# Kernel optimization log

Hardware: AMD Instinct MI355X
Metric: run time of the kernel (lower is better)

The kernel has to match this reference:

```python
import jax, jax.numpy as jnp
import numpy as np

N = 65536      # nodes
E = 524288     # edges (avg degree 8)
C = 128        # in_channels == hidden_channels
L = 3          # num_layers
EPS = 1e-5     # BatchNorm eps


def setup_inputs() -> dict:
    key = jax.random.key(0)
    ks = jax.random.split(key, 12)
    inv = 1.0 / np.sqrt(C)
    return {
        "x": jax.random.normal(ks[0], (N, C), jnp.float32),
        "edge_weight": jax.random.uniform(ks[1], (E,), jnp.float32),
        "bn_gamma": 1.0 + 0.1 * jax.random.normal(ks[2], (L, C), jnp.float32),
        "bn_beta": 0.1 * jax.random.normal(ks[3], (L, C), jnp.float32),
        "W_self": inv * jax.random.normal(ks[4], (L, C, C), jnp.float32),
        "W_neigh": inv * jax.random.normal(ks[5], (L, C, C), jnp.float32),
        "bias": 0.01 * jax.random.normal(ks[6], (L, C), jnp.float32),
        "lin_w": inv * jax.random.normal(ks[7], (C,), jnp.float32),
        "lin_b": 0.01 * jax.random.normal(ks[8], (), jnp.float32),
        "src": jax.random.randint(ks[9], (E,), 0, N),
        "dst": jax.random.randint(ks[10], (E,), 0, N),
    }


def reference(x, edge_weight, bn_gamma, bn_beta, W_self, W_neigh, bias, lin_w, lin_b, src, dst):
    # log1p on edge weights (done once in the torch module per layer; identical each layer)
    ew = jnp.log1p(edge_weight)[:, None]                     # [E,1]
    # in-degree for mean aggregation (DGL fn.mean); isolated nodes -> divide by 1 (sum is 0)
    deg = jax.ops.segment_sum(jnp.ones((E,), x.dtype), dst, num_segments=N)
    deg = jnp.maximum(deg, 1.0)[:, None]                     # [N,1]

    h = x
    for l in range(L):
        # BatchNorm1d over nodes (training-mode batch stats, biased variance)
        mu = jnp.mean(h, axis=0)
        var = jnp.mean((h - mu) ** 2, axis=0)
        h = (h - mu) * jax.lax.rsqrt(var + EPS) * bn_gamma[l] + bn_beta[l]
        # SAGEConv mean aggregator: msg = h[src] * w, neigh = mean over in-edges
        msg = h[src] * ew                                    # [E,C]
        neigh = jax.ops.segment_sum(msg, dst, num_segments=N) / deg  # [N,C]
        h = jax.nn.relu(h @ W_self[l] + neigh @ W_neigh[l] + bias[l])
    return h @ lin_w + lin_b                                 # [N]
```

## Files before the change

### kernel.cpp

```cpp
#include <hip/hip_runtime.h>
#include <hip/hip_fp16.h>

#define NN 65536
#define EE 524288
#define CC 128
#define CAP 32

typedef _Float16 f16x8 __attribute__((ext_vector_type(8)));
typedef float f32x4 __attribute__((ext_vector_type(4)));


__global__ void k_init(const float* __restrict__ x, __half* __restrict__ h,
                       float* __restrict__ pstat0,
                       const int* __restrict__ src, const int* __restrict__ dst,
                       const float* __restrict__ ew,
                       int* __restrict__ cnt, unsigned int* __restrict__ buf) {
    int b = blockIdx.x, t = threadIdx.x;
    if (b < 256) {
        const float4* xv = (const float4*)x;
        __half2* o = (__half2*)h;
        float s[4] = {0, 0, 0, 0}, q[4] = {0, 0, 0, 0};
        for (int k = 0; k < 32; k++) {
            int i = b * 8192 + k * 256 + t;
            float4 v = xv[i];
            o[2 * i]     = __floats2half2_rn(v.x, v.y);
            o[2 * i + 1] = __floats2half2_rn(v.z, v.w);
            s[0] += v.x; s[1] += v.y; s[2] += v.z; s[3] += v.w;
            q[0] += v.x * v.x; q[1] += v.y * v.y; q[2] += v.z * v.z; q[3] += v.w * v.w;
        }
        __shared__ float ls[256];
        ls[t] = 0.f;
        __syncthreads();
        int c0 = (t & 31) * 4;
#pragma unroll
        for (int u = 0; u < 4; u++) {
            atomicAdd(&ls[c0 + u], s[u]);
            atomicAdd(&ls[128 + c0 + u], q[u]);
        }
        __syncthreads();
        if (t < 128) {
            atomicAdd(&pstat0[t], ls[t]);
            atomicAdd(&pstat0[128 + t], ls[128 + t]);
        }
    } else {
        int base = (b - 256) * 1024 + t;
        int dd[4], sr[4];
        float we[4];
#pragma unroll
        for (int u = 0; u < 4; u++) dd[u] = dst[base + u * 256];
#pragma unroll
        for (int u = 0; u < 4; u++) sr[u] = src[base + u * 256];
#pragma unroll
        for (int u = 0; u < 4; u++) we[u] = ew[base + u * 256];
        int pos[4];
#pragma unroll
        for (int u = 0; u < 4; u++) pos[u] = atomicAdd(&cnt[dd[u]], 1);
#pragma unroll
        for (int u = 0; u < 4; u++) {
            float w = log1pf(we[u]);
            unsigned int pk = (unsigned int)sr[u] |
                              ((unsigned int)__half_as_ushort(__float2half(w)) << 16);
            if (pos[u] < CAP) buf[dd[u] * CAP + pos[u]] = pk;
        }
    }
}


__global__ void k_fold(const float* __restrict__ pstat_l,
                       const float* __restrict__ gamma, const float* __restrict__ beta,
                       const float* __restrict__ Ws, const float* __restrict__ Wn,
                       const float* __restrict__ bias,
                       __half* __restrict__ Wcat, float* __restrict__ crow,
                       float* __restrict__ cneigh) {
    int bid = blockIdx.x;
    int tid = threadIdx.x;
    int c = bid * 2 + (tid >> 7);
    int k = tid & 127;
    float mu = pstat_l[k] * (1.0f / NN);
    float var = pstat_l[128 + k] * (1.0f / NN) - mu * mu;
    float alpha = rsqrtf(var + 1e-5f) * gamma[k];
    float delta = beta[k] - mu * alpha;
    float ws = Ws[k * 128 + c];
    float wn = Wn[k * 128 + c];
    Wcat[c * 256 + k]       = __float2half(alpha * ws);
    Wcat[c * 256 + 128 + k] = __float2half(alpha * wn);
    float rs = delta * ws, rn = delta * wn;
#pragma unroll
    for (int off = 1; off < 64; off <<= 1) {
        rs += __shfl_xor(rs, off);
        rn += __shfl_xor(rn, off);
    }
    __shared__ float tmp[8];
    int wv = tid >> 6;
    if ((tid & 63) == 0) { tmp[wv * 2] = rs; tmp[wv * 2 + 1] = rn; }
    __syncthreads();
    if ((tid & 127) == 0) {
        int base = (tid >> 7) * 4;
        crow[c]   = bias[c] + tmp[base + 0] + tmp[base + 2];
        cneigh[c] = tmp[base + 1] + tmp[base + 3];
    }
}

__launch_bounds__(256, 4)
__global__ void k_layer(const __half* __restrict__ hin,
                        const int* __restrict__ cnt,
                        const unsigned int* __restrict__ buf,
                        const __half* __restrict__ Wcat,
                        const float* __restrict__ crow, const float* __restrict__ cneigh,
                        float* __restrict__ sod, int writeSod,
                        const float* __restrict__ lin_w, const float* __restrict__ lin_b,
                        __half* __restrict__ hout, float* __restrict__ outv, int mode,
                        float* __restrict__ pstatN) {
    __shared__ __half aggT[128 * 136];
    __shared__ float sodT[128];
    int tid = threadIdx.x;
    int lane = tid & 63;
    int wvid = tid >> 6;
    int l15 = lane & 15, quad = lane >> 4;
    int i0 = blockIdx.x * 128;
    int rbase = i0 + wvid * 32;

    f16x8 as0[4], as1[4];
#pragma unroll
    for (int s = 0; s < 4; s++) {
        int kof = s * 32 + quad * 8;
        as0[s] = *(const f16x8*)&hin[(rbase + l15) * 128 + kof];
        as1[s] = *(const f16x8*)&hin[(rbase + 16 + l15) * 128 + kof];
    }

    const __half2* h2 = (const __half2*)hin;
    int dv = 0;
    if (lane < 32) { dv = cnt[rbase + lane]; if (dv > CAP) dv = CAP; }
    int dA = __shfl(dv, 0), dB = __shfl(dv, 1);
    unsigned int pkA = 0, pkB = 0;
    if (lane < dA) pkA = buf[(rbase + 0) * CAP + lane];
    if (lane < dB) pkB = buf[(rbase + 1) * CAP + lane];

    for (int pair = 0; pair < 16; ++pair) {
        int ndA = 0, ndB = 0;
        unsigned int npA = 0, npB = 0;
        if (pair < 15) {
            ndA = __shfl(dv, 2 * pair + 2);
            ndB = __shfl(dv, 2 * pair + 3);
            if (lane < ndA) npA = buf[(rbase + 2 * pair + 2) * CAP + lane];
            if (lane < ndB) npB = buf[(rbase + 2 * pair + 3) * CAP + lane];
        }
        float ax[8], ay[8], bx[8], by[8];
#pragma unroll
        for (int u = 0; u < 8; u++) { ax[u] = 0.f; ay[u] = 0.f; bx[u] = 0.f; by[u] = 0.f; }
        int dmax = dA > dB ? dA : dB;
        int rounds = (dmax + 7) >> 3;
        for (int r = 0; r < rounds; r++) {
            int j = r * 8;
            unsigned int pA[8], pB[8];
            __half2 hA[8], hB[8];
#pragma unroll
            for (int u = 0; u < 8; u++) pA[u] = __shfl(pkA, j + u);
#pragma unroll
            for (int u = 0; u < 8; u++) pB[u] = __shfl(pkB, j + u);
#pragma unroll
            for (int u = 0; u < 8; u++) hA[u] = h2[(pA[u] & 0xFFFF) * 64 + lane];
#pragma unroll
            for (int u = 0; u < 8; u++) hB[u] = h2[(pB[u] & 0xFFFF) * 64 + lane];
#pragma unroll
            for (int u = 0; u < 8; u++) {
                float w = __half2float(__ushort_as_half((unsigned short)(pA[u] >> 16)));
                float2 v = __half22float2(hA[u]);
                ax[u] += w * v.x;
                ay[u] += w * v.y;
            }
#pragma unroll
            for (int u = 0; u < 8; u++) {
                float w = __half2float(__ushort_as_half((unsigned short)(pB[u] >> 16)));
                float2 v = __half22float2(hB[u]);
                bx[u] += w * v.x;
                by[u] += w * v.y;
            }
        }
        float axs = ((ax[0] + ax[1]) + (ax[2] + ax[3])) + ((ax[4] + ax[5]) + (ax[6] + ax[7]));
        float ays = ((ay[0] + ay[1]) + (ay[2] + ay[3])) + ((ay[4] + ay[5]) + (ay[6] + ay[7]));
        float bxs = ((bx[0] + bx[1]) + (bx[2] + bx[3])) + ((bx[4] + bx[5]) + (bx[6] + bx[7]));
        float bys = ((by[0] + by[1]) + (by[2] + by[3])) + ((by[4] + by[5]) + (by[6] + by[7]));
        float invA = 1.0f / (float)(dA > 1 ? dA : 1);
        float invB = 1.0f / (float)(dB > 1 ? dB : 1);
        int rloc = wvid * 32 + 2 * pair;
        *(__half2*)&aggT[rloc * 136 + 2 * lane]       = __floats2half2_rn(axs * invA, ays * invA);
        *(__half2*)&aggT[(rloc + 1) * 136 + 2 * lane] = __floats2half2_rn(bxs * invB, bys * invB);
        if (writeSod) {
            float wA = __half2float(__ushort_as_half((unsigned short)(pkA >> 16)));
            float wB = __half2float(__ushort_as_half((unsigned short)(pkB >> 16)));
#pragma unroll
            for (int off = 1; off < 64; off <<= 1) {
                wA += __shfl_xor(wA, off);
                wB += __shfl_xor(wB, off);
            }
            if (lane == 0) {
                sodT[rloc] = wA * invA;     sod[i0 + rloc] = wA * invA;
                sodT[rloc + 1] = wB * invB; sod[i0 + rloc + 1] = wB * invB;
            }
        }
        dA = ndA; dB = ndB; pkA = npA; pkB = npB;
    }

    f32x4 acc0[8], acc1[8];
    f32x4 zero = {0.f, 0.f, 0.f, 0.f};
#pragma unroll
    for (int t = 0; t < 8; t++) { acc0[t] = zero; acc1[t] = zero; }

#pragma unroll
    for (int s = 0; s < 4; s++) {
        int kof = s * 32 + quad * 8;
#pragma unroll
        for (int tn = 0; tn < 8; tn++) {
            f16x8 bf = *(const f16x8*)&Wcat[(tn * 16 + l15) * 256 + kof];
            acc0[tn] = __builtin_amdgcn_mfma_f32_16x16x32_f16(as0[s], bf, acc0[tn], 0, 0, 0);
            acc1[tn] = __builtin_amdgcn_mfma_f32_16x16x32_f16(as1[s], bf, acc1[tn], 0, 0, 0);
        }
    }
#pragma unroll
    for (int s = 0; s < 4; s++) {
        int kof = s * 32 + quad * 8;
        f16x8 an0 = *(const f16x8*)&aggT[(wvid * 32 + l15) * 136 + kof];
        f16x8 an1 = *(const f16x8*)&aggT[(wvid * 32 + 16 + l15) * 136 + kof];
#pragma unroll
        for (int tn = 0; tn < 8; tn++) {
            f16x8 bf = *(const f16x8*)&Wcat[(tn * 16 + l15) * 256 + 128 + kof];
            acc0[tn] = __builtin_amdgcn_mfma_f32_16x16x32_f16(an0, bf, acc0[tn], 0, 0, 0);
            acc1[tn] = __builtin_amdgcn_mfma_f32_16x16x32_f16(an1, bf, acc1[tn], 0, 0, 0);
        }
    }

    float cr[8], cn[8];
#pragma unroll
    for (int tn = 0; tn < 8; tn++) {
        cr[tn] = crow[tn * 16 + l15];
        cn[tn] = cneigh[tn * 16 + l15];
    }
    int rwbase = i0 + wvid * 32 + quad * 4;

    if (mode == 0) {
        float cs[8], cq[8];
#pragma unroll
        for (int tn = 0; tn < 8; tn++) { cs[tn] = 0.f; cq[tn] = 0.f; }
#pragma unroll
        for (int tm = 0; tm < 2; tm++) {
#pragma unroll
            for (int r = 0; r < 4; r++) {
                int row = rwbase + tm * 16 + r;
                float sdv = writeSod ? sodT[row - i0] : sod[row];
#pragma unroll
                for (int tn = 0; tn < 8; tn++) {
                    float v = (tm ? acc1[tn][r] : acc0[tn][r]) + cr[tn] + sdv * cn[tn];
                    v = fmaxf(v, 0.f);
                    hout[row * 128 + tn * 16 + l15] = __float2half(v);
                    cs[tn] += v;
                    cq[tn] += v * v;
                }
            }
        }
#pragma unroll
        for (int tn = 0; tn < 8; tn++) {
            cs[tn] += __shfl_xor(cs[tn], 16); cs[tn] += __shfl_xor(cs[tn], 32);
            cq[tn] += __shfl_xor(cq[tn], 16); cq[tn] += __shfl_xor(cq[tn], 32);
        }
        float* st = (float*)aggT;
        __syncthreads();
        st[tid] = 0.f;
        __syncthreads();
        if (lane < 16) {
#pragma unroll
            for (int tn = 0; tn < 8; tn++) {
                atomicAdd(&st[tn * 16 + l15], cs[tn]);
                atomicAdd(&st[128 + tn * 16 + l15], cq[tn]);
            }
        }
        __syncthreads();
        if (tid < 128) {
            atomicAdd(&pstatN[tid], st[tid]);
            atomicAdd(&pstatN[128 + tid], st[128 + tid]);
        }
    } else {
        float lw[8];
#pragma unroll
        for (int tn = 0; tn < 8; tn++) lw[tn] = lin_w[tn * 16 + l15];
        float lb = lin_b[0];
#pragma unroll
        for (int tm = 0; tm < 2; tm++) {
#pragma unroll
            for (int r = 0; r < 4; r++) {
                int row = rwbase + tm * 16 + r;
                float sdv = sod[row];
                float p = 0.f;
#pragma unroll
                for (int tn = 0; tn < 8; tn++) {
                    float v = (tm ? acc1[tn][r] : acc0[tn][r]) + cr[tn] + sdv * cn[tn];
                    v = fmaxf(v, 0.f);
                    p += v * lw[tn];
                }
                p += __shfl_xor(p, 1);
                p += __shfl_xor(p, 2);
                p += __shfl_xor(p, 4);
                p += __shfl_xor(p, 8);
                if (l15 == 0) outv[row] = p + lb;
            }
        }
    }
}


extern "C" void kernel_launch(void* const* d_in, const int* in_sizes, int n_in,
                              void* d_out, int out_size, void* d_ws, size_t ws_size,
                              hipStream_t stream) {
    (void)in_sizes; (void)n_in; (void)out_size; (void)ws_size;
    const float* x     = (const float*)d_in[0];
    const float* ew    = (const float*)d_in[1];
    const float* gamma = (const float*)d_in[2];
    const float* beta  = (const float*)d_in[3];
    const float* Ws    = (const float*)d_in[4];
    const float* Wn    = (const float*)d_in[5];
    const float* bias  = (const float*)d_in[6];
    const float* lin_w = (const float*)d_in[7];
    const float* lin_b = (const float*)d_in[8];
    const int*   srcI  = (const int*)d_in[9];
    const int*   dstI  = (const int*)d_in[10];
    float* out = (float*)d_out;

    char* p = (char*)d_ws;
    __half* ha   = (__half*)p; p += (size_t)NN * CC * 2;
    __half* hb   = (__half*)p; p += (size_t)NN * CC * 2;
    __half* Wcat = (__half*)p; p += 256 * 128 * 2;
    float* crow   = (float*)p; p += 512;
    float* cneigh = (float*)p; p += 512;
    float* sod    = (float*)p; p += (size_t)NN * 4;
    unsigned int* buf = (unsigned int*)p; p += (size_t)NN * CAP * 4;
    int*   cnt    = (int*)p;   p += (size_t)NN * 4;
    float* pstat  = (float*)p; p += 3 * 256 * 4;

    hipMemsetAsync(cnt, 0, (size_t)NN * 4 + 3 * 256 * 4, stream);

    k_init<<<dim3(256 + EE / 1024), dim3(256), 0, stream>>>(x, ha, pstat, srcI, dstI, ew, cnt, buf);

    const __half* hin = ha;
    __half* hout = hb;
    for (int l = 0; l < 3; l++) {
        k_fold<<<dim3(64), dim3(256), 0, stream>>>(
            pstat + l * 256, gamma + l * CC, beta + l * CC,
            Ws + (size_t)l * CC * CC, Wn + (size_t)l * CC * CC, bias + l * CC,
            Wcat, crow, cneigh);
        int mode = (l == 2) ? 1 : 0;
        float* pstatN = (mode == 0) ? (pstat + (l + 1) * 256) : pstat;
        k_layer<<<dim3(NN / 128), dim3(256), 0, stream>>>(
            hin, cnt, buf, Wcat, crow, cneigh, sod, (l == 0) ? 1 : 0,
            lin_w, lin_b, hout, out, mode, pstatN);
        const __half* t = hin; hin = hout; hout = (__half*)t;
    }
}
```

Baseline: 301.2 us.

## Halve rows per layer block and bucket BatchNorm stat atomics

```diff
diff --git a/kernel.cpp b/kernel.cpp
--- a/kernel.cpp
+++ b/kernel.cpp
@@ -5,6 +5,8 @@
 #define EE 524288
 #define CC 128
 #define CAP 32
+#define RPB 64
+#define NBUCK 8
 
 typedef _Float16 f16x8 __attribute__((ext_vector_type(8)));
 typedef float f32x4 __attribute__((ext_vector_type(4)));
@@ -76,8 +78,14 @@
     int tid = threadIdx.x;
     int c = bid * 2 + (tid >> 7);
     int k = tid & 127;
-    float mu = pstat_l[k] * (1.0f / NN);
-    float var = pstat_l[128 + k] * (1.0f / NN) - mu * mu;
+    float su = 0.f, sq = 0.f;
+#pragma unroll
+    for (int b = 0; b < NBUCK; b++) {
+        su += pstat_l[b * 256 + k];
+        sq += pstat_l[b * 256 + 128 + k];
+    }
+    float mu = su * (1.0f / NN);
+    float var = sq * (1.0f / NN) - mu * mu;
     float alpha = rsqrtf(var + 1e-5f) * gamma[k];
     float delta = beta[k] - mu * alpha;
     float ws = Ws[k * 128 + c];
@@ -111,35 +119,34 @@
                         const float* __restrict__ lin_w, const float* __restrict__ lin_b,
                         __half* __restrict__ hout, float* __restrict__ outv, int mode,
                         float* __restrict__ pstatN) {
-    __shared__ __half aggT[128 * 136];
-    __shared__ float sodT[128];
+    __shared__ __half aggT[RPB * 136];
+    __shared__ float sodT[RPB];
     int tid = threadIdx.x;
     int lane = tid & 63;
     int wvid = tid >> 6;
     int l15 = lane & 15, quad = lane >> 4;
-    int i0 = blockIdx.x * 128;
-    int rbase = i0 + wvid * 32;
-
-    f16x8 as0[4], as1[4];
+    int i0 = blockIdx.x * RPB;
+    int rbase = i0 + wvid * 16;
+
+    f16x8 as0[4];
 #pragma unroll
     for (int s = 0; s < 4; s++) {
         int kof = s * 32 + quad * 8;
         as0[s] = *(const f16x8*)&hin[(rbase + l15) * 128 + kof];
-        as1[s] = *(const f16x8*)&hin[(rbase + 16 + l15) * 128 + kof];
     }
 
     const __half2* h2 = (const __half2*)hin;
     int dv = 0;
-    if (lane < 32) { dv = cnt[rbase + lane]; if (dv > CAP) dv = CAP; }
+    if (lane < 16) { dv = cnt[rbase + lane]; if (dv > CAP) dv = CAP; }
     int dA = __shfl(dv, 0), dB = __shfl(dv, 1);
     unsigned int pkA = 0, pkB = 0;
     if (lane < dA) pkA = buf[(rbase + 0) * CAP + lane];
     if (lane < dB) pkB = buf[(rbase + 1) * CAP + lane];
 
-    for (int pair = 0; pair < 16; ++pair) {
+    for (int pair = 0; pair < 8; ++pair) {
         int ndA = 0, ndB = 0;
         unsigned int npA = 0, npB = 0;
-        if (pair < 15) {
+        if (pair < 7) {
             ndA = __shfl(dv, 2 * pair + 2);
             ndB = __shfl(dv, 2 * pair + 3);
             if (lane < ndA) npA = buf[(rbase + 2 * pair + 2) * CAP + lane];
@@ -183,7 +190,7 @@
         float bys = ((by[0] + by[1]) + (by[2] + by[3])) + ((by[4] + by[5]) + (by[6] + by[7]));
         float invA = 1.0f / (float)(dA > 1 ? dA : 1);
         float invB = 1.0f / (float)(dB > 1 ? dB : 1);
-        int rloc = wvid * 32 + 2 * pair;
+        int rloc = wvid * 16 + 2 * pair;
         *(__half2*)&aggT[rloc * 136 + 2 * lane]       = __floats2half2_rn(axs * invA, ays * invA);
         *(__half2*)&aggT[(rloc + 1) * 136 + 2 * lane] = __floats2half2_rn(bxs * invB, bys * invB);
         if (writeSod) {
@@ -202,10 +209,10 @@
         dA = ndA; dB = ndB; pkA = npA; pkB = npB;
     }
 
-    f32x4 acc0[8], acc1[8];
+    f32x4 acc[8];
     f32x4 zero = {0.f, 0.f, 0.f, 0.f};
 #pragma unroll
-    for (int t = 0; t < 8; t++) { acc0[t] = zero; acc1[t] = zero; }
+    for (int t = 0; t < 8; t++) acc[t] = zero;
 
 #pragma unroll
     for (int s = 0; s < 4; s++) {
@@ -213,20 +220,17 @@
 #pragma unroll
         for (int tn = 0; tn < 8; tn++) {
             f16x8 bf = *(const f16x8*)&Wcat[(tn * 16 + l15) * 256 + kof];
-            acc0[tn] = __builtin_amdgcn_mfma_f32_16x16x32_f16(as0[s], bf, acc0[tn], 0, 0, 0);
-            acc1[tn] = __builtin_amdgcn_mfma_f32_16x16x32_f16(as1[s], bf, acc1[tn], 0, 0, 0);
+            acc[tn] = __builtin_amdgcn_mfma_f32_16x16x32_f16(as0[s], bf, acc[tn], 0, 0, 0);
         }
     }
 #pragma unroll
     for (int s = 0; s < 4; s++) {
         int kof = s * 32 + quad * 8;
-        f16x8 an0 = *(const f16x8*)&aggT[(wvid * 32 + l15) * 136 + kof];
-        f16x8 an1 = *(const f16x8*)&aggT[(wvid * 32 + 16 + l15) * 136 + kof];
+        f16x8 an0 = *(const f16x8*)&aggT[(wvid * 16 + l15) * 136 + kof];
 #pragma unroll
         for (int tn = 0; tn < 8; tn++) {
             f16x8 bf = *(const f16x8*)&Wcat[(tn * 16 + l15) * 256 + 128 + kof];
-            acc0[tn] = __builtin_amdgcn_mfma_f32_16x16x32_f16(an0, bf, acc0[tn], 0, 0, 0);
-            acc1[tn] = __builtin_amdgcn_mfma_f32_16x16x32_f16(an1, bf, acc1[tn], 0, 0, 0);
+            acc[tn] = __builtin_amdgcn_mfma_f32_16x16x32_f16(an0, bf, acc[tn], 0, 0, 0);
         }
     }
 
@@ -236,26 +240,23 @@
         cr[tn] = crow[tn * 16 + l15];
         cn[tn] = cneigh[tn * 16 + l15];
     }
-    int rwbase = i0 + wvid * 32 + quad * 4;
+    int rwbase = i0 + wvid * 16 + quad * 4;
 
     if (mode == 0) {
         float cs[8], cq[8];
 #pragma unroll
         for (int tn = 0; tn < 8; tn++) { cs[tn] = 0.f; cq[tn] = 0.f; }
 #pragma unroll
-        for (int tm = 0; tm < 2; tm++) {
-#pragma unroll
-            for (int r = 0; r < 4; r++) {
-                int row = rwbase + tm * 16 + r;
-                float sdv = writeSod ? sodT[row - i0] : sod[row];
-#pragma unroll
-                for (int tn = 0; tn < 8; tn++) {
-                    float v = (tm ? acc1[tn][r] : acc0[tn][r]) + cr[tn] + sdv * cn[tn];
-                    v = fmaxf(v, 0.f);
-                    hout[row * 128 + tn * 16 + l15] = __float2half(v);
-                    cs[tn] += v;
-                    cq[tn] += v * v;
-                }
+        for (int r = 0; r < 4; r++) {
+            int row = rwbase + r;
+            float sdv = writeSod ? sodT[row - i0] : sod[row];
+#pragma unroll
+            for (int tn = 0; tn < 8; tn++) {
+                float v = acc[tn][r] + cr[tn] + sdv * cn[tn];
+                v = fmaxf(v, 0.f);
+                hout[row * 128 + tn * 16 + l15] = __float2half(v);
+                cs[tn] += v;
+                cq[tn] += v * v;
             }
         }
 #pragma unroll
@@ -276,8 +277,9 @@
         }
         __syncthreads();
         if (tid < 128) {
-            atomicAdd(&pstatN[tid], st[tid]);
-            atomicAdd(&pstatN[128 + tid], st[128 + tid]);
+            float* pb = pstatN + ((blockIdx.x & (NBUCK - 1)) << 8);
+            atomicAdd(&pb[tid], st[tid]);
+            atomicAdd(&pb[128 + tid], st[128 + tid]);
         }
     } else {
         float lw[8];
@@ -285,24 +287,21 @@
         for (int tn = 0; tn < 8; tn++) lw[tn] = lin_w[tn * 16 + l15];
         float lb = lin_b[0];
 #pragma unroll
-        for (int tm = 0; tm < 2; tm++) {
-#pragma unroll
-            for (int r = 0; r < 4; r++) {
-                int row = rwbase + tm * 16 + r;
-                float sdv = sod[row];
-                float p = 0.f;
-#pragma unroll
-                for (int tn = 0; tn < 8; tn++) {
-                    float v = (tm ? acc1[tn][r] : acc0[tn][r]) + cr[tn] + sdv * cn[tn];
-                    v = fmaxf(v, 0.f);
-                    p += v * lw[tn];
-                }
-                p += __shfl_xor(p, 1);
-                p += __shfl_xor(p, 2);
-                p += __shfl_xor(p, 4);
-                p += __shfl_xor(p, 8);
-                if (l15 == 0) outv[row] = p + lb;
-            }
+        for (int r = 0; r < 4; r++) {
+            int row = rwbase + r;
+            float sdv = sod[row];
+            float p = 0.f;
+#pragma unroll
+            for (int tn = 0; tn < 8; tn++) {
+                float v = acc[tn][r] + cr[tn] + sdv * cn[tn];
+                v = fmaxf(v, 0.f);
+                p += v * lw[tn];
+            }
+            p += __shfl_xor(p, 1);
+            p += __shfl_xor(p, 2);
+            p += __shfl_xor(p, 4);
+            p += __shfl_xor(p, 8);
+            if (l15 == 0) outv[row] = p + lb;
         }
     }
 }
@@ -334,9 +333,9 @@
     float* sod    = (float*)p; p += (size_t)NN * 4;
     unsigned int* buf = (unsigned int*)p; p += (size_t)NN * CAP * 4;
     int*   cnt    = (int*)p;   p += (size_t)NN * 4;
-    float* pstat  = (float*)p; p += 3 * 256 * 4;
-
-    hipMemsetAsync(cnt, 0, (size_t)NN * 4 + 3 * 256 * 4, stream);
+    float* pstat  = (float*)p; p += 3 * NBUCK * 256 * 4;
+
+    hipMemsetAsync(cnt, 0, (size_t)NN * 4 + 3 * NBUCK * 256 * 4, stream);
 
     k_init<<<dim3(256 + EE / 1024), dim3(256), 0, stream>>>(x, ha, pstat, srcI, dstI, ew, cnt, buf);
 
@@ -344,12 +343,12 @@
     __half* hout = hb;
     for (int l = 0; l < 3; l++) {
         k_fold<<<dim3(64), dim3(256), 0, stream>>>(
-            pstat + l * 256, gamma + l * CC, beta + l * CC,
+            pstat + (size_t)l * NBUCK * 256, gamma + l * CC, beta + l * CC,
             Ws + (size_t)l * CC * CC, Wn + (size_t)l * CC * CC, bias + l * CC,
             Wcat, crow, cneigh);
         int mode = (l == 2) ? 1 : 0;
-        float* pstatN = (mode == 0) ? (pstat + (l + 1) * 256) : pstat;
-        k_layer<<<dim3(NN / 128), dim3(256), 0, stream>>>(
+        float* pstatN = (mode == 0) ? (pstat + (size_t)(l + 1) * NBUCK * 256) : pstat;
+        k_layer<<<dim3(NN / RPB), dim3(256), 0, stream>>>(
             hin, cnt, buf, Wcat, crow, cneigh, sod, (l == 0) ? 1 : 0,
             lin_w, lin_b, hout, out, mode, pstatN);
         const __half* t = hin; hin = hout; hout = (__half*)t;
```

New measurement: 293.0 us. -2.7%, faster.
